# Kernel optimization log

Hardware: AMD Instinct MI355X
Metric: run time of the kernel (lower is better)

Reference implementation:

```python
import jax, jax.numpy as jnp
import numpy as np
import math

B, NTOK, NH, D = 8, 1000, 8, 64
CHUNK = 8  # query-chunk size for the pairwise L1 score computation


def _linearm(w, x):
    # LinearM: w [out, in+1] (last column is bias); x [b, t, in] -> [b, t, out]
    return jnp.einsum('oi,bti->bto', w[:, :-1], x) + w[:, -1]


def setup_inputs() -> dict:
    key = jax.random.key(0)
    ks = jax.random.split(key, 4)
    scl = 0.005
    x = jax.random.normal(ks[0], (B, NTOK, D), dtype=jnp.float32)
    wq = (scl * jax.random.normal(ks[1], (NH * D, D + 1), dtype=jnp.float32)).at[:, -1].set(0.0)
    wv = (scl * jax.random.normal(ks[2], (NH * D, D + 1), dtype=jnp.float32)).at[:, -1].set(0.0)
    wk = scl * jnp.ones((NH, D), dtype=jnp.float32)
    wf = (scl * jax.random.normal(ks[3], (D, D + 1), dtype=jnp.float32)).at[:, -1].set(0.0)
    return {"x": x, "wq": wq, "wv": wv, "wk": wk, "wf": wf}


def _forward(x, wq, wv, wk, wf):
    b, t, d = x.shape
    nh = wk.shape[0]
    scale = 1.0 / math.sqrt(d)

    q = _linearm(wq, x).reshape(b, t, nh, d)          # [b, t, nh, d]
    v = _linearm(wv, x).reshape(b, t, nh, d)          # [b, t, nh, d]
    k = x[:, :, None, :] * wk[None, None]             # [b, t, nh, d]

    # L1-distance attention scores: a[b, s, q, h] = -scale * sum_w |q[b,q,h,w] - k[b,s,h,w]|
    # Computed in query chunks so the [b, t, t, nh, d] pairwise tensor is never materialized.
    nc = t // CHUNK
    qc = q.reshape(b, nc, CHUNK, nh, d).transpose(1, 0, 2, 3, 4)  # [nc, b, C, nh, d]

    @jax.checkpoint
    def scores(qch):
        # qch: [b, C, nh, d] -> [b, t(src), C, nh]
        return -scale * jnp.sum(jnp.abs(qch[:, None] - k[:, :, None]), axis=-1)

    a = jax.lax.map(scores, qc)                       # [nc, b, t, C, nh]
    a = a.transpose(1, 2, 0, 3, 4).reshape(b, t, t, nh)  # [b, src, dst, nh]

    # Extra all-zero "null" source row (mirrors a[:, a2len, :, :] = 0 before softmax)
    a = jnp.concatenate([a, jnp.zeros((b, 1, t, nh), a.dtype)], axis=1)
    a = jax.nn.softmax(a, axis=1)[:, :t]              # softmax over sources, drop null row

    # einsum('bsdh,bshw->bdhw') followed by sum over heads, fused:
    out = jnp.einsum('bsth,bshw->btw', a, v)          # [b, t, d]

    y = jax.nn.relu(out)                              # self.gelu is actually ReLU
    y = _linearm(wf, y)
    return x + y


def reference(x, wq, wv, wk, wf):
    return _forward(x, wq, wv, wk, wf)
```

## Files before the change

### kernel.cpp

```cpp
#include <hip/hip_runtime.h>
#include <math.h>

#define Bb 8
#define Tt 1000
#define TPAD 1024
#define NHh 8
#define Dd 64

typedef short bf16x8 __attribute__((ext_vector_type(8)));
typedef float f32x4 __attribute__((ext_vector_type(4)));

#define QOFF (-0.3f)
#define QSTEP (0.6f / 256.0f)
#define QINV (256.0f / 0.6f)
#define CQ (-0.125f * 1.44269504088896341f * QSTEP)

__device__ __forceinline__ unsigned sad_u8(unsigned a, unsigned b, unsigned c) {
#if __has_builtin(__builtin_amdgcn_sad_u8)
    return __builtin_amdgcn_sad_u8(a, b, c);
#else
    unsigned d;
    asm("v_sad_u8 %0, %1, %2, %3" : "=v"(d) : "v"(a), "v"(b), "v"(c));
    return d;
#endif
}

__device__ __forceinline__ unsigned quant8(float v) {
    float t = (v - QOFF) * QINV + 0.5f;
    t = fminf(fmaxf(t, 0.0f), 255.0f);
    return (unsigned)(int)t;
}

__device__ __forceinline__ unsigned cvt_pk_bf16(float lo, float hi) {
    unsigned r;
    asm("v_cvt_pk_bf16_f32 %0, %1, %2" : "=v"(r) : "v"(lo), "v"(hi));
    return r;
}

__device__ __forceinline__ bf16x8 mkbf(unsigned u0, unsigned u1, unsigned u2, unsigned u3) {
    union { unsigned u[4]; bf16x8 v; } x;
    x.u[0] = u0; x.u[1] = u1; x.u[2] = u2; x.u[3] = u3;
    return x.v;
}

__device__ __forceinline__ bf16x8 bfc(uint4 q) {
    union { uint4 q; bf16x8 v; } x; x.q = q; return x.v;
}

#define GLDS(gsrc, ldst) \
    __builtin_amdgcn_global_load_lds((const __attribute__((address_space(1))) unsigned*)(gsrc), \
                                     (__attribute__((address_space(3))) unsigned*)(ldst), 16, 0, 0)

__global__ __launch_bounds__(256) void prep_kernel(
    const float* __restrict__ x, const float* __restrict__ wq,
    const float* __restrict__ wv, const float* __restrict__ wk,
    unsigned* __restrict__ qq8, unsigned* __restrict__ kq8,
    uint4* __restrict__ vfrag)
{
    __shared__ float xs[64][68];
    __shared__ float ws[64][65];
    __shared__ float vS[64][68];
    const int tid = threadIdx.x;
    const int st = blockIdx.x;
    const int cb = blockIdx.y;
    const int b  = blockIdx.z;
    const bool isQ = (cb < 8);
    const int h = isQ ? cb : (cb - 8);
    const float* W = isQ ? wq : wv;
    const int cBase = h * 64;
    const int bh = b * NHh + h;

#pragma unroll
    for (int i = 0; i < 4; ++i) {
        int f4 = tid + i * 256;
        int r = f4 >> 4, c4 = (f4 & 15) << 2;
        int row = st * 64 + r; if (row >= Tt) row = Tt - 1;
        *(float4*)&xs[r][c4] = *(const float4*)&x[((size_t)b * Tt + row) * 64 + c4];
    }
#pragma unroll
    for (int i = 0; i < 16; ++i) {
        int idx = tid + i * 256;
        int c = idx >> 6, k = idx & 63;
        ws[c][k] = W[(cBase + c) * 65 + k];
    }
    __syncthreads();

    const int rg = tid >> 4, cg = tid & 15;
    const int r0 = rg * 4, c0 = cg * 4;
    float acc[4][4];
#pragma unroll
    for (int j = 0; j < 4; ++j) {
        float bias = W[(cBase + c0 + j) * 65 + 64];
#pragma unroll
        for (int i = 0; i < 4; ++i) acc[i][j] = bias;
    }
    for (int k0 = 0; k0 < 64; k0 += 4) {
        float4 a[4];
#pragma unroll
        for (int i = 0; i < 4; ++i) a[i] = *(const float4*)&xs[r0 + i][k0];
#pragma unroll
        for (int j = 0; j < 4; ++j) {
            float b0 = ws[c0 + j][k0 + 0];
            float b1 = ws[c0 + j][k0 + 1];
            float b2 = ws[c0 + j][k0 + 2];
            float b3 = ws[c0 + j][k0 + 3];
#pragma unroll
            for (int i = 0; i < 4; ++i)
                acc[i][j] += a[i].x * b0 + a[i].y * b1 + a[i].z * b2 + a[i].w * b3;
        }
    }

    if (isQ) {
#pragma unroll
        for (int i = 0; i < 4; ++i) {
            int t = st * 64 + r0 + i;
            unsigned d = 0u;
            if (t < Tt)
                d = quant8(acc[i][0]) | (quant8(acc[i][1]) << 8) |
                    (quant8(acc[i][2]) << 16) | (quant8(acc[i][3]) << 24);
            qq8[((size_t)bh * TPAD + t) * 16 + cg] = d;
        }
        {
            const int r = tid >> 2, c4 = tid & 3;
            const int t = st * 64 + r;
            unsigned kd[4];
            if (t < Tt) {
#pragma unroll
                for (int dw = 0; dw < 4; ++dw) {
                    int w = c4 * 16 + dw * 4;
                    float4 wkv = *(const float4*)&wk[h * 64 + w];
                    kd[dw] = quant8(xs[r][w + 0] * wkv.x) |
                             (quant8(xs[r][w + 1] * wkv.y) << 8) |
                             (quant8(xs[r][w + 2] * wkv.z) << 16) |
                             (quant8(xs[r][w + 3] * wkv.w) << 24);
                }
            } else {
                kd[0] = kd[1] = kd[2] = kd[3] = 0u;
            }
            const int c4s = c4 ^ ((r >> 3) & 3);
            *(uint4*)&kq8[((size_t)bh * TPAD + t) * 16 + c4s * 4] =
                make_uint4(kd[0], kd[1], kd[2], kd[3]);
        }
    } else {
#pragma unroll
        for (int i = 0; i < 4; ++i) {
            float4 o; o.x = acc[i][0]; o.y = acc[i][1]; o.z = acc[i][2]; o.w = acc[i][3];
            *(float4*)&vS[r0 + i][c0] = o;
        }
        __syncthreads();
#pragma unroll
        for (int e2 = 0; e2 < 2; ++e2) {
            int ent = tid + e2 * 256;
            int kk = ent >> 8, rem = ent & 255, n = rem >> 6, lane = rem & 63;
            int ts = kk * 32 + ((lane >> 4) << 3);
            int w  = n * 16 + (lane & 15);
            unsigned o[4];
#pragma unroll
            for (int pr = 0; pr < 4; ++pr) {
                int t0 = st * 64 + ts + pr * 2;
                float lo = (t0 < Tt)     ? vS[ts + pr * 2][w]     : 0.0f;
                float hi = (t0 + 1 < Tt) ? vS[ts + pr * 2 + 1][w] : 0.0f;
                o[pr] = cvt_pk_bf16(lo, hi);
            }
            vfrag[(((size_t)bh * 16 + st) * 8 + (kk * 4 + n)) * 64 + lane] =
                make_uint4(o[0], o[1], o[2], o[3]);
        }
    }
}

__global__ __launch_bounds__(256) void attn_kernel(
    const unsigned* __restrict__ qq8, const unsigned* __restrict__ kq8,
    const uint4* __restrict__ vfrag, float* __restrict__ part)
{
    __shared__ unsigned kS[3][1024];
    __shared__ uint4    vS[3][512];

    const int tid = threadIdx.x;
    const int wv_ = tid >> 6;
    const int l   = tid & 63;
    const int g   = l >> 4;
    const int m   = l & 15;
    const int qt  = blockIdx.x;
    const int h   = blockIdx.y, b = blockIdx.z;
    const int bh  = b * NHh + h;

    unsigned qv[16];
    {
        const uint4* qp = (const uint4*)(qq8 + ((size_t)bh * TPAD + qt * 64 + wv_ * 16 + m) * 16);
        *(uint4*)&qv[0]  = qp[0];
        *(uint4*)&qv[4]  = qp[1];
        *(uint4*)&qv[8]  = qp[2];
        *(uint4*)&qv[12] = qp[3];
    }

    const uint4* kg = (const uint4*)kq8 + (size_t)bh * 4096;
    const uint4* vg = vfrag + (size_t)bh * 8192;

#define STAGE(TT, SB) do { \
        const uint4* kt_ = kg + (TT) * 256; \
        const uint4* vt_ = vg + (TT) * 512; \
        GLDS(kt_ + wv_ * 64 + l,       &kS[SB][(wv_ * 64) * 4]); \
        GLDS(vt_ + wv_ * 128 + l,      &vS[SB][wv_ * 128]); \
        GLDS(vt_ + wv_ * 128 + 64 + l, &vS[SB][wv_ * 128 + 64]); \
    } while (0)

    STAGE(0, 0);
    STAGE(1, 1);
    asm volatile("s_waitcnt vmcnt(3)" ::: "memory");
    __builtin_amdgcn_s_barrier();
    __builtin_amdgcn_sched_barrier(0);

    f32x4 acc0 = {0.f,0.f,0.f,0.f}, acc1 = acc0, acc2 = acc0, acc3 = acc0;
    float dsum = 0.0f;

    int cur = 0, stb = 2;
#pragma unroll 1
    for (int t = 0; t < 16; ++t) {
        if (t < 14) STAGE(t + 2, stb);

        bf16x8 A0, A1;
#pragma unroll
        for (int kk = 0; kk < 2; ++kk) {
            unsigned accu[8];
#pragma unroll
            for (int e = 0; e < 8; ++e) {
                const unsigned* kb = &kS[cur][(kk * 32 + (g << 3) + e) << 4];
                uint4 c0 = *(const uint4*)(kb + ((0 ^ g) << 2));
                uint4 c1 = *(const uint4*)(kb + ((1 ^ g) << 2));
                uint4 c2 = *(const uint4*)(kb + ((2 ^ g) << 2));
                uint4 c3 = *(const uint4*)(kb + ((3 ^ g) << 2));
                const unsigned* k0 = (const unsigned*)&c0;
                const unsigned* k1 = (const unsigned*)&c1;
                const unsigned* k2 = (const unsigned*)&c2;
                const unsigned* k3 = (const unsigned*)&c3;
                unsigned sa = 0u, sb = 0u;
#pragma unroll
                for (int w = 0; w < 4; ++w) sa = sad_u8(qv[w],      k0[w], sa);
#pragma unroll
                for (int w = 0; w < 4; ++w) sb = sad_u8(qv[4 + w],  k1[w], sb);
#pragma unroll
                for (int w = 0; w < 4; ++w) sa = sad_u8(qv[8 + w],  k2[w], sa);
#pragma unroll
                for (int w = 0; w < 4; ++w) sb = sad_u8(qv[12 + w], k3[w], sb);
                accu[e] = sa + sb;
            }
            const bool maskall = (t == 15) && (kk == 1) && (g >= 1);
            float p[8];
#pragma unroll
            for (int e = 0; e < 8; ++e) {
                p[e] = maskall ? 0.0f : __builtin_amdgcn_exp2f(CQ * (float)accu[e]);
                dsum += p[e];
            }
            bf16x8 A = mkbf(cvt_pk_bf16(p[0], p[1]), cvt_pk_bf16(p[2], p[3]),
                            cvt_pk_bf16(p[4], p[5]), cvt_pk_bf16(p[6], p[7]));
            if (kk == 0) A0 = A; else A1 = A;
        }

        {
            uint4 vf0 = vS[cur][0 * 64 + l], vf1 = vS[cur][1 * 64 + l];
            uint4 vf2 = vS[cur][2 * 64 + l], vf3 = vS[cur][3 * 64 + l];
            acc0 = __builtin_amdgcn_mfma_f32_16x16x32_bf16(A0, bfc(vf0), acc0, 0, 0, 0);
            acc1 = __builtin_amdgcn_mfma_f32_16x16x32_bf16(A0, bfc(vf1), acc1, 0, 0, 0);
            acc2 = __builtin_amdgcn_mfma_f32_16x16x32_bf16(A0, bfc(vf2), acc2, 0, 0, 0);
            acc3 = __builtin_amdgcn_mfma_f32_16x16x32_bf16(A0, bfc(vf3), acc3, 0, 0, 0);
        }
        {
            uint4 vf4 = vS[cur][4 * 64 + l], vf5 = vS[cur][5 * 64 + l];
            uint4 vf6 = vS[cur][6 * 64 + l], vf7 = vS[cur][7 * 64 + l];
            acc0 = __builtin_amdgcn_mfma_f32_16x16x32_bf16(A1, bfc(vf4), acc0, 0, 0, 0);
            acc1 = __builtin_amdgcn_mfma_f32_16x16x32_bf16(A1, bfc(vf5), acc1, 0, 0, 0);
            acc2 = __builtin_amdgcn_mfma_f32_16x16x32_bf16(A1, bfc(vf6), acc2, 0, 0, 0);
            acc3 = __builtin_amdgcn_mfma_f32_16x16x32_bf16(A1, bfc(vf7), acc3, 0, 0, 0);
        }

        if (t < 14) {
            asm volatile("s_waitcnt vmcnt(3)" ::: "memory");
        } else if (t == 14) {
            asm volatile("s_waitcnt vmcnt(0)" ::: "memory");
        }
        if (t < 15) {
            __builtin_amdgcn_s_barrier();
            __builtin_amdgcn_sched_barrier(0);
        }
        cur = (cur == 2) ? 0 : cur + 1;
        stb = (stb == 2) ? 0 : stb + 1;
    }
#undef STAGE

    dsum += __shfl_xor(dsum, 16);
    dsum += __shfl_xor(dsum, 32);
    const float den = 1.0f + dsum;

#pragma unroll
    for (int j = 0; j < 4; ++j) {
        float dj = __shfl(den, g * 4 + j);
        int row = qt * 64 + wv_ * 16 + g * 4 + j;
        if (row < Tt) {
            float inv = 1.0f / dj;
            float* o = part + (((size_t)b * Tt + row) * NHh + h) * 64 + m;
            o[0]  = acc0[j] * inv;
            o[16] = acc1[j] * inv;
            o[32] = acc2[j] * inv;
            o[48] = acc3[j] * inv;
        }
    }
}

__global__ __launch_bounds__(256) void finalize_kernel(
    const float* __restrict__ x, const float* __restrict__ wf,
    const float* __restrict__ part, float* __restrict__ out)
{
    __shared__ float wfs[64][65];
    __shared__ float osh[4][64];
    const int tid = threadIdx.x;
    for (int i = tid; i < 64 * 65; i += 256) wfs[i / 65][i % 65] = wf[i];
    const int wave = tid >> 6, lane = tid & 63;
    const int token = blockIdx.x * 4 + wave;
    float o = 0.f;
    const float* pt = part + (size_t)token * NHh * Dd;
#pragma unroll
    for (int hh = 0; hh < NHh; ++hh) o += pt[hh * Dd + lane];
    o = fmaxf(o, 0.f);
    osh[wave][lane] = o;
    __syncthreads();
    float acc = wfs[lane][64];
#pragma unroll 8
    for (int w = 0; w < 64; ++w) acc += wfs[lane][w] * osh[wave][w];
    out[(size_t)token * Dd + lane] = x[(size_t)token * Dd + lane] + acc;
}

extern "C" void kernel_launch(void* const* d_in, const int* in_sizes, int n_in,
                              void* d_out, int out_size, void* d_ws, size_t ws_size,
                              hipStream_t stream)
{
    const float* x  = (const float*)d_in[0];
    const float* wq = (const float*)d_in[1];
    const float* wv = (const float*)d_in[2];
    const float* wk = (const float*)d_in[3];
    const float* wf = (const float*)d_in[4];
    float* out = (float*)d_out;

    char* base = (char*)d_ws;
    float*    part  = (float*)base;
    unsigned* qq8   = (unsigned*)(base + 16384000);
    unsigned* kq8   = (unsigned*)(base + 16384000 + 4194304);
    uint4*    vfrag = (uint4*)(base + 16384000 + 2 * 4194304);

    prep_kernel<<<dim3(16, 16, Bb), 256, 0, stream>>>(x, wq, wv, wk, qq8, kq8, vfrag);
    attn_kernel<<<dim3(16, NHh, Bb), 256, 0, stream>>>(qq8, kq8, vfrag, part);
    finalize_kernel<<<2000, 256, 0, stream>>>(x, wf, part, out);
}
```

Before: 96.46 us.

## Split attention over source halves with per-wave key tiles and in-block reduction

```diff
diff --git a/kernel.cpp b/kernel.cpp
--- a/kernel.cpp
+++ b/kernel.cpp
@@ -35,6 +35,14 @@
     unsigned r;
     asm("v_cvt_pk_bf16_f32 %0, %1, %2" : "=v"(r) : "v"(lo), "v"(hi));
     return r;
+}
+
+__device__ __forceinline__ unsigned short f2bf(float v) {
+    return (unsigned short)(cvt_pk_bf16(v, v) & 0xffffu);
+}
+
+__device__ __forceinline__ float bf2f(unsigned short u) {
+    union { unsigned u; float f; } x; x.u = ((unsigned)u) << 16; return x.f;
 }
 
 __device__ __forceinline__ bf16x8 mkbf(unsigned u0, unsigned u1, unsigned u2, unsigned u3) {
@@ -170,10 +178,11 @@
 
 __global__ __launch_bounds__(256) void attn_kernel(
     const unsigned* __restrict__ qq8, const unsigned* __restrict__ kq8,
-    const uint4* __restrict__ vfrag, float* __restrict__ part)
+    const uint4* __restrict__ vfrag,
+    unsigned short* __restrict__ numbf, float* __restrict__ dsums)
 {
-    __shared__ unsigned kS[3][1024];
-    __shared__ uint4    vS[3][512];
+    __shared__ uint4 smem[2048];
+    __shared__ float dredx[4][4][16];
 
     const int tid = threadIdx.x;
     const int wv_ = tid >> 6;
@@ -181,134 +190,199 @@
     const int g   = l >> 4;
     const int m   = l & 15;
     const int qt  = blockIdx.x;
-    const int h   = blockIdx.y, b = blockIdx.z;
+    const int h   = blockIdx.y;
+    const int bz  = blockIdx.z;
+    const int b   = bz >> 1;
+    const int half = bz & 1;
     const int bh  = b * NHh + h;
-
-    unsigned qv[16];
+    const int tb  = half * 8 + wv_ * 2;
+
+    unsigned qA[16], qB[16], qC[16], qD[16];
     {
-        const uint4* qp = (const uint4*)(qq8 + ((size_t)bh * TPAD + qt * 64 + wv_ * 16 + m) * 16);
-        *(uint4*)&qv[0]  = qp[0];
-        *(uint4*)&qv[4]  = qp[1];
-        *(uint4*)&qv[8]  = qp[2];
-        *(uint4*)&qv[12] = qp[3];
+        const uint4* qp = (const uint4*)qq8 + ((size_t)bh * TPAD + qt * 64 + m) * 4;
+        *(uint4*)&qA[0] = qp[0];       *(uint4*)&qA[4] = qp[1];
+        *(uint4*)&qA[8] = qp[2];       *(uint4*)&qA[12] = qp[3];
+        *(uint4*)&qB[0] = qp[64];      *(uint4*)&qB[4] = qp[65];
+        *(uint4*)&qB[8] = qp[66];      *(uint4*)&qB[12] = qp[67];
+        *(uint4*)&qC[0] = qp[128];     *(uint4*)&qC[4] = qp[129];
+        *(uint4*)&qC[8] = qp[130];     *(uint4*)&qC[12] = qp[131];
+        *(uint4*)&qD[0] = qp[192];     *(uint4*)&qD[4] = qp[193];
+        *(uint4*)&qD[8] = qp[194];     *(uint4*)&qD[12] = qp[195];
     }
 
     const uint4* kg = (const uint4*)kq8 + (size_t)bh * 4096;
     const uint4* vg = vfrag + (size_t)bh * 8192;
 
-#define STAGE(TT, SB) do { \
-        const uint4* kt_ = kg + (TT) * 256; \
-        const uint4* vt_ = vg + (TT) * 512; \
-        GLDS(kt_ + wv_ * 64 + l,       &kS[SB][(wv_ * 64) * 4]); \
-        GLDS(vt_ + wv_ * 128 + l,      &vS[SB][wv_ * 128]); \
-        GLDS(vt_ + wv_ * 128 + 64 + l, &vS[SB][wv_ * 128 + 64]); \
-    } while (0)
-
-    STAGE(0, 0);
-    STAGE(1, 1);
-    asm volatile("s_waitcnt vmcnt(3)" ::: "memory");
-    __builtin_amdgcn_s_barrier();
+    uint4* kw = &smem[wv_ * 512];
+    {
+#pragma unroll
+        for (int c = 0; c < 4; ++c) GLDS(kg + tb * 256 + c * 64 + l,       &kw[c * 64]);
+#pragma unroll
+        for (int c = 0; c < 4; ++c) GLDS(kg + (tb + 1) * 256 + c * 64 + l, &kw[256 + c * 64]);
+    }
+    asm volatile("s_waitcnt vmcnt(0)" ::: "memory");
     __builtin_amdgcn_sched_barrier(0);
 
-    f32x4 acc0 = {0.f,0.f,0.f,0.f}, acc1 = acc0, acc2 = acc0, acc3 = acc0;
-    float dsum = 0.0f;
-
-    int cur = 0, stb = 2;
-#pragma unroll 1
-    for (int t = 0; t < 16; ++t) {
-        if (t < 14) STAGE(t + 2, stb);
-
-        bf16x8 A0, A1;
+    f32x4 accA[4], accB[4], accC[4], accD[4];
+#pragma unroll
+    for (int n = 0; n < 4; ++n) {
+        accA[n] = (f32x4){0.f,0.f,0.f,0.f};
+        accB[n] = accA[n]; accC[n] = accA[n]; accD[n] = accA[n];
+    }
+    float dsA = 0.f, dsB = 0.f, dsC = 0.f, dsD = 0.f;
+
+#pragma unroll
+    for (int ti = 0; ti < 2; ++ti) {
+        const int t = tb + ti;
+        const uint4* kbase = &kw[ti * 256];
+        const uint4* vt = vg + (size_t)t * 512 + l;
+
 #pragma unroll
         for (int kk = 0; kk < 2; ++kk) {
-            unsigned accu[8];
+            uint4 vf0 = vt[(kk * 4 + 0) * 64];
+            uint4 vf1 = vt[(kk * 4 + 1) * 64];
+            uint4 vf2 = vt[(kk * 4 + 2) * 64];
+            uint4 vf3 = vt[(kk * 4 + 3) * 64];
+
+            const bool maskall = (t == 15) && (kk == 1) && (g >= 1);
+            unsigned waA[4], waB[4], waC[4], waD[4];
+            float pvA, pvB, pvC, pvD;
 #pragma unroll
             for (int e = 0; e < 8; ++e) {
-                const unsigned* kb = &kS[cur][(kk * 32 + (g << 3) + e) << 4];
-                uint4 c0 = *(const uint4*)(kb + ((0 ^ g) << 2));
-                uint4 c1 = *(const uint4*)(kb + ((1 ^ g) << 2));
-                uint4 c2 = *(const uint4*)(kb + ((2 ^ g) << 2));
-                uint4 c3 = *(const uint4*)(kb + ((3 ^ g) << 2));
+                const uint4* kb = kbase + ((kk * 32 + (g << 3) + e) << 2);
+                uint4 c0 = kb[0 ^ g], c1 = kb[1 ^ g], c2 = kb[2 ^ g], c3 = kb[3 ^ g];
                 const unsigned* k0 = (const unsigned*)&c0;
                 const unsigned* k1 = (const unsigned*)&c1;
                 const unsigned* k2 = (const unsigned*)&c2;
                 const unsigned* k3 = (const unsigned*)&c3;
-                unsigned sa = 0u, sb = 0u;
-#pragma unroll
-                for (int w = 0; w < 4; ++w) sa = sad_u8(qv[w],      k0[w], sa);
-#pragma unroll
-                for (int w = 0; w < 4; ++w) sb = sad_u8(qv[4 + w],  k1[w], sb);
-#pragma unroll
-                for (int w = 0; w < 4; ++w) sa = sad_u8(qv[8 + w],  k2[w], sa);
-#pragma unroll
-                for (int w = 0; w < 4; ++w) sb = sad_u8(qv[12 + w], k3[w], sb);
-                accu[e] = sa + sb;
+                unsigned sA0 = 0u, sA1 = 0u, sB0 = 0u, sB1 = 0u;
+                unsigned sC0 = 0u, sC1 = 0u, sD0 = 0u, sD1 = 0u;
+#pragma unroll
+                for (int w = 0; w < 4; ++w) {
+                    sA0 = sad_u8(qA[w],     k0[w], sA0); sA1 = sad_u8(qA[4 + w], k1[w], sA1);
+                    sB0 = sad_u8(qB[w],     k0[w], sB0); sB1 = sad_u8(qB[4 + w], k1[w], sB1);
+                    sC0 = sad_u8(qC[w],     k0[w], sC0); sC1 = sad_u8(qC[4 + w], k1[w], sC1);
+                    sD0 = sad_u8(qD[w],     k0[w], sD0); sD1 = sad_u8(qD[4 + w], k1[w], sD1);
+                }
+#pragma unroll
+                for (int w = 0; w < 4; ++w) {
+                    sA0 = sad_u8(qA[8 + w], k2[w], sA0); sA1 = sad_u8(qA[12 + w], k3[w], sA1);
+                    sB0 = sad_u8(qB[8 + w], k2[w], sB0); sB1 = sad_u8(qB[12 + w], k3[w], sB1);
+                    sC0 = sad_u8(qC[8 + w], k2[w], sC0); sC1 = sad_u8(qC[12 + w], k3[w], sC1);
+                    sD0 = sad_u8(qD[8 + w], k2[w], sD0); sD1 = sad_u8(qD[12 + w], k3[w], sD1);
+                }
+                float pA = maskall ? 0.f : __builtin_amdgcn_exp2f(CQ * (float)(sA0 + sA1));
+                float pB = maskall ? 0.f : __builtin_amdgcn_exp2f(CQ * (float)(sB0 + sB1));
+                float pC = maskall ? 0.f : __builtin_amdgcn_exp2f(CQ * (float)(sC0 + sC1));
+                float pD = maskall ? 0.f : __builtin_amdgcn_exp2f(CQ * (float)(sD0 + sD1));
+                dsA += pA; dsB += pB; dsC += pC; dsD += pD;
+                if (e & 1) {
+                    waA[e >> 1] = cvt_pk_bf16(pvA, pA);
+                    waB[e >> 1] = cvt_pk_bf16(pvB, pB);
+                    waC[e >> 1] = cvt_pk_bf16(pvC, pC);
+                    waD[e >> 1] = cvt_pk_bf16(pvD, pD);
+                } else { pvA = pA; pvB = pB; pvC = pC; pvD = pD; }
             }
-            const bool maskall = (t == 15) && (kk == 1) && (g >= 1);
-            float p[8];
-#pragma unroll
-            for (int e = 0; e < 8; ++e) {
-                p[e] = maskall ? 0.0f : __builtin_amdgcn_exp2f(CQ * (float)accu[e]);
-                dsum += p[e];
-            }
-            bf16x8 A = mkbf(cvt_pk_bf16(p[0], p[1]), cvt_pk_bf16(p[2], p[3]),
-                            cvt_pk_bf16(p[4], p[5]), cvt_pk_bf16(p[6], p[7]));
-            if (kk == 0) A0 = A; else A1 = A;
-        }
-
-        {
-            uint4 vf0 = vS[cur][0 * 64 + l], vf1 = vS[cur][1 * 64 + l];
-            uint4 vf2 = vS[cur][2 * 64 + l], vf3 = vS[cur][3 * 64 + l];
-            acc0 = __builtin_amdgcn_mfma_f32_16x16x32_bf16(A0, bfc(vf0), acc0, 0, 0, 0);
-            acc1 = __builtin_amdgcn_mfma_f32_16x16x32_bf16(A0, bfc(vf1), acc1, 0, 0, 0);
-            acc2 = __builtin_amdgcn_mfma_f32_16x16x32_bf16(A0, bfc(vf2), acc2, 0, 0, 0);
-            acc3 = __builtin_amdgcn_mfma_f32_16x16x32_bf16(A0, bfc(vf3), acc3, 0, 0, 0);
-        }
-        {
-            uint4 vf4 = vS[cur][4 * 64 + l], vf5 = vS[cur][5 * 64 + l];
-            uint4 vf6 = vS[cur][6 * 64 + l], vf7 = vS[cur][7 * 64 + l];
-            acc0 = __builtin_amdgcn_mfma_f32_16x16x32_bf16(A1, bfc(vf4), acc0, 0, 0, 0);
-            acc1 = __builtin_amdgcn_mfma_f32_16x16x32_bf16(A1, bfc(vf5), acc1, 0, 0, 0);
-            acc2 = __builtin_amdgcn_mfma_f32_16x16x32_bf16(A1, bfc(vf6), acc2, 0, 0, 0);
-            acc3 = __builtin_amdgcn_mfma_f32_16x16x32_bf16(A1, bfc(vf7), acc3, 0, 0, 0);
-        }
-
-        if (t < 14) {
-            asm volatile("s_waitcnt vmcnt(3)" ::: "memory");
-        } else if (t == 14) {
-            asm volatile("s_waitcnt vmcnt(0)" ::: "memory");
-        }
-        if (t < 15) {
-            __builtin_amdgcn_s_barrier();
-            __builtin_amdgcn_sched_barrier(0);
-        }
-        cur = (cur == 2) ? 0 : cur + 1;
-        stb = (stb == 2) ? 0 : stb + 1;
-    }
-#undef STAGE
-
-    dsum += __shfl_xor(dsum, 16);
-    dsum += __shfl_xor(dsum, 32);
-    const float den = 1.0f + dsum;
-
-#pragma unroll
-    for (int j = 0; j < 4; ++j) {
-        float dj = __shfl(den, g * 4 + j);
-        int row = qt * 64 + wv_ * 16 + g * 4 + j;
-        if (row < Tt) {
-            float inv = 1.0f / dj;
-            float* o = part + (((size_t)b * Tt + row) * NHh + h) * 64 + m;
-            o[0]  = acc0[j] * inv;
-            o[16] = acc1[j] * inv;
-            o[32] = acc2[j] * inv;
-            o[48] = acc3[j] * inv;
-        }
-    }
+            bf16x8 AA = mkbf(waA[0], waA[1], waA[2], waA[3]);
+            bf16x8 AB = mkbf(waB[0], waB[1], waB[2], waB[3]);
+            bf16x8 AC = mkbf(waC[0], waC[1], waC[2], waC[3]);
+            bf16x8 AD = mkbf(waD[0], waD[1], waD[2], waD[3]);
+
+            accA[0] = __builtin_amdgcn_mfma_f32_16x16x32_bf16(AA, bfc(vf0), accA[0], 0, 0, 0);
+            accB[0] = __builtin_amdgcn_mfma_f32_16x16x32_bf16(AB, bfc(vf0), accB[0], 0, 0, 0);
+            accC[0] = __builtin_amdgcn_mfma_f32_16x16x32_bf16(AC, bfc(vf0), accC[0], 0, 0, 0);
+            accD[0] = __builtin_amdgcn_mfma_f32_16x16x32_bf16(AD, bfc(vf0), accD[0], 0, 0, 0);
+            accA[1] = __builtin_amdgcn_mfma_f32_16x16x32_bf16(AA, bfc(vf1), accA[1], 0, 0, 0);
+            accB[1] = __builtin_amdgcn_mfma_f32_16x16x32_bf16(AB, bfc(vf1), accB[1], 0, 0, 0);
+            accC[1] = __builtin_amdgcn_mfma_f32_16x16x32_bf16(AC, bfc(vf1), accC[1], 0, 0, 0);
+            accD[1] = __builtin_amdgcn_mfma_f32_16x16x32_bf16(AD, bfc(vf1), accD[1], 0, 0, 0);
+            accA[2] = __builtin_amdgcn_mfma_f32_16x16x32_bf16(AA, bfc(vf2), accA[2], 0, 0, 0);
+            accB[2] = __builtin_amdgcn_mfma_f32_16x16x32_bf16(AB, bfc(vf2), accB[2], 0, 0, 0);
+            accC[2] = __builtin_amdgcn_mfma_f32_16x16x32_bf16(AC, bfc(vf2), accC[2], 0, 0, 0);
+            accD[2] = __builtin_amdgcn_mfma_f32_16x16x32_bf16(AD, bfc(vf2), accD[2], 0, 0, 0);
+            accA[3] = __builtin_amdgcn_mfma_f32_16x16x32_bf16(AA, bfc(vf3), accA[3], 0, 0, 0);
+            accB[3] = __builtin_amdgcn_mfma_f32_16x16x32_bf16(AB, bfc(vf3), accB[3], 0, 0, 0);
+            accC[3] = __builtin_amdgcn_mfma_f32_16x16x32_bf16(AC, bfc(vf3), accC[3], 0, 0, 0);
+            accD[3] = __builtin_amdgcn_mfma_f32_16x16x32_bf16(AD, bfc(vf3), accD[3], 0, 0, 0);
+        }
+    }
+
+    dsA += __shfl_xor(dsA, 16); dsA += __shfl_xor(dsA, 32);
+    dsB += __shfl_xor(dsB, 16); dsB += __shfl_xor(dsB, 32);
+    dsC += __shfl_xor(dsC, 16); dsC += __shfl_xor(dsC, 32);
+    dsD += __shfl_xor(dsD, 16); dsD += __shfl_xor(dsD, 32);
+
+    __syncthreads();
+
+    f32x4* red = (f32x4*)smem;
+    if (l < 16) {
+        dredx[wv_][0][l] = dsA; dredx[wv_][1][l] = dsB;
+        dredx[wv_][2][l] = dsC; dredx[wv_][3][l] = dsD;
+    }
+
+#define PUB(SLOT) do { \
+        _Pragma("unroll") for (int n = 0; n < 4; ++n) { \
+            red[(SLOT) * 1024 + (0 * 4 + n) * 64 + l] = accA[n]; \
+            red[(SLOT) * 1024 + (1 * 4 + n) * 64 + l] = accB[n]; \
+            red[(SLOT) * 1024 + (2 * 4 + n) * 64 + l] = accC[n]; \
+            red[(SLOT) * 1024 + (3 * 4 + n) * 64 + l] = accD[n]; \
+        } } while (0)
+#define ADD(SLOT) do { \
+        _Pragma("unroll") for (int n = 0; n < 4; ++n) { \
+            f32x4 ra = red[(SLOT) * 1024 + (0 * 4 + n) * 64 + l]; \
+            f32x4 rb = red[(SLOT) * 1024 + (1 * 4 + n) * 64 + l]; \
+            f32x4 rc = red[(SLOT) * 1024 + (2 * 4 + n) * 64 + l]; \
+            f32x4 rd = red[(SLOT) * 1024 + (3 * 4 + n) * 64 + l]; \
+            _Pragma("unroll") for (int j = 0; j < 4; ++j) { \
+                accA[n][j] += ra[j]; accB[n][j] += rb[j]; \
+                accC[n][j] += rc[j]; accD[n][j] += rd[j]; } \
+        } } while (0)
+
+    if (wv_ & 1) PUB(wv_ >> 1);
+    __syncthreads();
+    if (!(wv_ & 1)) ADD(wv_ >> 1);
+    __syncthreads();
+    if (wv_ == 2) PUB(0);
+    __syncthreads();
+    if (wv_ == 0) {
+        ADD(0);
+        float dT0 = dredx[0][0][m] + dredx[1][0][m] + dredx[2][0][m] + dredx[3][0][m];
+        float dT1 = dredx[0][1][m] + dredx[1][1][m] + dredx[2][1][m] + dredx[3][1][m];
+        float dT2 = dredx[0][2][m] + dredx[1][2][m] + dredx[2][2][m] + dredx[3][2][m];
+        float dT3 = dredx[0][3][m] + dredx[1][3][m] + dredx[2][3][m] + dredx[3][3][m];
+
+#define STOREROW(ACC, RS) do { \
+        _Pragma("unroll") for (int j = 0; j < 4; ++j) { \
+            int row = qt * 64 + (RS) * 16 + g * 4 + j; \
+            if (row < Tt) { \
+                unsigned short* o = numbf + (((size_t)(b * Tt + row) * 16) + h * 2 + half) * 64 + m; \
+                o[0]  = f2bf(ACC[0][j]); \
+                o[16] = f2bf(ACC[1][j]); \
+                o[32] = f2bf(ACC[2][j]); \
+                o[48] = f2bf(ACC[3][j]); \
+            } } } while (0)
+        STOREROW(accA, 0);
+        STOREROW(accB, 1);
+        STOREROW(accC, 2);
+        STOREROW(accD, 3);
+#undef STOREROW
+        if (l < 16) {
+            int r0_ = qt * 64 + m,      r1_ = qt * 64 + 16 + m;
+            int r2_ = qt * 64 + 32 + m, r3_ = qt * 64 + 48 + m;
+            if (r0_ < Tt) dsums[(((size_t)(b * Tt + r0_) * 8) + h) * 2 + half] = dT0;
+            if (r1_ < Tt) dsums[(((size_t)(b * Tt + r1_) * 8) + h) * 2 + half] = dT1;
+            if (r2_ < Tt) dsums[(((size_t)(b * Tt + r2_) * 8) + h) * 2 + half] = dT2;
+            if (r3_ < Tt) dsums[(((size_t)(b * Tt + r3_) * 8) + h) * 2 + half] = dT3;
+        }
+    }
+#undef PUB
+#undef ADD
 }
 
 __global__ __launch_bounds__(256) void finalize_kernel(
     const float* __restrict__ x, const float* __restrict__ wf,
-    const float* __restrict__ part, float* __restrict__ out)
+    const unsigned short* __restrict__ numbf, const float* __restrict__ dsums,
+    float* __restrict__ out)
 {
     __shared__ float wfs[64][65];
     __shared__ float osh[4][64];
@@ -316,10 +390,18 @@
     for (int i = tid; i < 64 * 65; i += 256) wfs[i / 65][i % 65] = wf[i];
     const int wave = tid >> 6, lane = tid & 63;
     const int token = blockIdx.x * 4 + wave;
+
+    const float dsv = dsums[(size_t)token * 16 + (lane & 15)];
+    const unsigned short* np = numbf + (size_t)token * 1024;
     float o = 0.f;
-    const float* pt = part + (size_t)token * NHh * Dd;
-#pragma unroll
-    for (int hh = 0; hh < NHh; ++hh) o += pt[hh * Dd + lane];
+#pragma unroll
+    for (int hh = 0; hh < 8; ++hh) {
+        float den = 1.0f + __shfl(dsv, 2 * hh) + __shfl(dsv, 2 * hh + 1);
+        float inv = 1.0f / den;
+        float a0 = bf2f(np[(2 * hh) * 64 + lane]);
+        float a1 = bf2f(np[(2 * hh + 1) * 64 + lane]);
+        o += (a0 + a1) * inv;
+    }
     o = fmaxf(o, 0.f);
     osh[wave][lane] = o;
     __syncthreads();
@@ -341,12 +423,13 @@
     float* out = (float*)d_out;
 
     char* base = (char*)d_ws;
-    float*    part  = (float*)base;
-    unsigned* qq8   = (unsigned*)(base + 16384000);
-    unsigned* kq8   = (unsigned*)(base + 16384000 + 4194304);
-    uint4*    vfrag = (uint4*)(base + 16384000 + 2 * 4194304);
+    unsigned short* numbf = (unsigned short*)base;
+    float*    dsums = (float*)(base + 16384000);
+    unsigned* qq8   = (unsigned*)(base + 16896000);
+    unsigned* kq8   = (unsigned*)(base + 16896000 + 4194304);
+    uint4*    vfrag = (uint4*)(base + 16896000 + 2 * 4194304);
 
     prep_kernel<<<dim3(16, 16, Bb), 256, 0, stream>>>(x, wq, wv, wk, qq8, kq8, vfrag);
-    attn_kernel<<<dim3(16, NHh, Bb), 256, 0, stream>>>(qq8, kq8, vfrag, part);
-    finalize_kernel<<<2000, 256, 0, stream>>>(x, wf, part, out);
-}
+    attn_kernel<<<dim3(16, NHh, 2 * Bb), 256, 0, stream>>>(qq8, kq8, vfrag, numbf, dsums);
+    finalize_kernel<<<2000, 256, 0, stream>>>(x, wf, numbf, dsums, out);
+}
```

Result: slower. 129.0 us (+33.7%).
